# Kernel optimization log

Hardware: AMD Instinct MI355X
Metric: run time of the kernel (lower is better)

The kernel has to match this reference:

```python
import jax, jax.numpy as jnp
import numpy as np

N_NODES = 50000
N_EDGES = 150000
NODE_F, EDGE_F = 4, 11
HID, HID_OUT = 512, 1024
VS, AS_, N_ACT = 2048, 2048, 1000


def _graph_conv(x, W, b, src, dst, n, edge_weight=None):
    # DGL GraphConv, norm='both': D_out^{-1/2} on src feats, sum-aggregate, D_in^{-1/2} on dst.
    deg_out = jnp.maximum(jnp.zeros((n,), x.dtype).at[src].add(1.0), 1.0)
    deg_in = jnp.maximum(jnp.zeros((n,), x.dtype).at[dst].add(1.0), 1.0)
    h = x * (deg_out[:, None] ** -0.5)
    mult_first = W.shape[0] > W.shape[1]
    if mult_first:
        h = h @ W
    m = h[src]  # [E, d] gather
    if edge_weight is not None:
        m = m * edge_weight  # elementwise u_mul_e
    agg = jax.ops.segment_sum(m, dst, num_segments=n)
    if not mult_first:
        agg = agg @ W
    return agg * (deg_in[:, None] ** -0.5) + b


def setup_inputs() -> dict:
    key = jax.random.key(0)
    ks = jax.random.split(key, 16)
    s = 0.05
    return {
        'node_feats': jax.random.normal(ks[0], (N_NODES, NODE_F), jnp.float32),
        'edge_feats': jax.random.normal(ks[1], (N_EDGES, EDGE_F), jnp.float32),
        'W1': jax.random.normal(ks[2], (NODE_F, EDGE_F), jnp.float32) * s,
        'b1': jnp.zeros((EDGE_F,), jnp.float32),
        'W2': jax.random.normal(ks[3], (EDGE_F, HID), jnp.float32) * s,
        'b2': jnp.zeros((HID,), jnp.float32),
        'W3': jax.random.normal(ks[4], (HID, HID_OUT), jnp.float32) * s,
        'b3': jnp.zeros((HID_OUT,), jnp.float32),
        'Wv1': jax.random.normal(ks[5], (HID_OUT, VS), jnp.float32) * s,
        'bv1': jnp.zeros((VS,), jnp.float32),
        'Wv2': jax.random.normal(ks[6], (VS, 1), jnp.float32) * s,
        'bv2': jnp.zeros((1,), jnp.float32),
        'Wa1': jax.random.normal(ks[7], (HID_OUT, AS_), jnp.float32) * s,
        'ba1': jnp.zeros((AS_,), jnp.float32),
        'Wa2': jax.random.normal(ks[8], (AS_, N_ACT), jnp.float32) * s,
        'ba2': jnp.zeros((N_ACT,), jnp.float32),
        'src': jax.random.randint(ks[9], (N_EDGES,), 0, N_NODES, jnp.int32),
        'dst': jax.random.randint(ks[10], (N_EDGES,), 0, N_NODES, jnp.int32),
    }


def reference(node_feats, edge_feats, W1, b1, W2, b2, W3, b3,
              Wv1, bv1, Wv2, bv2, Wa1, ba1, Wa2, ba2, src, dst):
    n = node_feats.shape[0]
    loop = jnp.arange(n, dtype=src.dtype)
    srcL = jnp.concatenate([src, loop])  # add_self_loop
    dstL = jnp.concatenate([dst, loop])
    # self-loop edges get zero edge features (DGL default)
    ef = jnp.concatenate([edge_feats, jnp.zeros((n, edge_feats.shape[1]), edge_feats.dtype)], axis=0)

    h = jax.nn.relu(_graph_conv(node_feats, W1, b1, srcL, dstL, n))          # [N, 11]
    h = jax.nn.relu(_graph_conv(h, W2, b2, srcL, dstL, n, edge_weight=ef))   # [N, 512]
    h = _graph_conv(h, W3, b3, srcL, dstL, n)                                # [N, 1024]

    g_emb = jnp.mean(h, axis=0, keepdims=True)  # dgl.mean_nodes, single graph -> [1, 1024]

    v = jax.nn.relu(g_emb @ Wv1 + bv1) @ Wv2 + bv2        # [1, 1]
    a = jax.nn.relu(g_emb @ Wa1 + ba1) @ Wa2 + ba2        # [1, N_ACT]
    return v + (a - a.mean())
```

## Files before the change

kernel.cpp:

```cpp
#include <hip/hip_runtime.h>

#define NN 50000
#define NE 150000
#define NB 196

__global__ __launch_bounds__(256) void k_deg(const int* __restrict__ src,
                                             const int* __restrict__ dst,
                                             int* __restrict__ deg_out,
                                             int* __restrict__ deg_in) {
    int e = blockIdx.x * 256 + threadIdx.x;
    if (e < NE) {
        atomicAdd(&deg_out[src[e]], 1);
        atomicAdd(&deg_in[dst[e]], 1);
    }
}

__global__ __launch_bounds__(256) void k_bsum(const int* __restrict__ deg_in,
                                              int* __restrict__ bsum_in) {
    __shared__ int si[256];
    int t = threadIdx.x;
    int idx = blockIdx.x * 256 + t;
    si[t] = (idx < NN) ? deg_in[idx] : 0;
    __syncthreads();
    for (int off = 128; off >= 1; off >>= 1) {
        if (t < off) si[t] += si[t + off];
        __syncthreads();
    }
    if (t == 0) bsum_in[blockIdx.x] = si[0];
}

__global__ __launch_bounds__(256) void k_rowptr(const int* __restrict__ deg_in,
                                                const int* __restrict__ deg_out,
                                                const int* __restrict__ bsum_in,
                                                const float* __restrict__ x,
                                                int* __restrict__ rp_in,
                                                float* __restrict__ dins,
                                                float* __restrict__ douts,
                                                float4* __restrict__ xs4) {
    __shared__ int si[256];
    int b = blockIdx.x, t = threadIdx.x;
    si[t] = (t < b) ? bsum_in[t] : 0;
    __syncthreads();
    for (int off = 128; off >= 1; off >>= 1) {
        if (t < off) si[t] += si[t + off];
        __syncthreads();
    }
    int off_in = si[0];
    __syncthreads();
    int idx = b * 256 + t;
    int di = (idx < NN) ? deg_in[idx] : 0;
    si[t] = di;
    __syncthreads();
    for (int off = 1; off < 256; off <<= 1) {
        int a = (t >= off) ? si[t - off] : 0;
        __syncthreads();
        si[t] += a;
        __syncthreads();
    }
    if (idx < NN) {
        rp_in[idx] = off_in + si[t] - di;
        float dif = rsqrtf((float)(di + 1));
        float dqf = rsqrtf((float)(deg_out[idx] + 1));
        dins[idx] = dif;
        douts[idx] = dqf;
        float4 x4 = ((const float4*)x)[idx];
        x4.x *= dqf; x4.y *= dqf; x4.z *= dqf; x4.w *= dqf;
        xs4[idx] = x4;
    }
    if (b == 0 && t == 0) rp_in[NN] = NE;
}

__global__ __launch_bounds__(256) void k_scatter(const int* __restrict__ src,
                                                 const int* __restrict__ dst,
                                                 const float* __restrict__ ef,
                                                 const int* __restrict__ rp_in,
                                                 const float* __restrict__ dins,
                                                 int* __restrict__ cur_in,
                                                 int2* __restrict__ ndcsr,
                                                 float4* __restrict__ ef4,
                                                 float* __restrict__ c) {
    int e = blockIdx.x * 256 + threadIdx.x;
    if (e >= NE) return;
    int s = src[e], d = dst[e];
    int pi = rp_in[d] + atomicAdd(&cur_in[d], 1);
    ndcsr[pi] = make_int2(s, d);
    const float* er = ef + (size_t)e * 11;
    ef4[(size_t)pi * 3 + 0] = make_float4(er[0], er[1], er[2], er[3]);
    ef4[(size_t)pi * 3 + 1] = make_float4(er[4], er[5], er[6], er[7]);
    ef4[(size_t)pi * 3 + 2] = make_float4(er[8], er[9], er[10], 0.f);
    atomicAdd(&c[s], dins[d]);
}

__global__ __launch_bounds__(256) void k_conv1g(const float4* __restrict__ xs4,
                                                const int2* __restrict__ ndcsr,
                                                const int* __restrict__ rp_in,
                                                const float* __restrict__ dins,
                                                const float* __restrict__ douts,
                                                const float* __restrict__ W1,
                                                const float* __restrict__ b1,
                                                float4* __restrict__ h1s4) {
    int n = blockIdx.x * 256 + threadIdx.x;
    if (n >= NN) return;
    float din  = dins[n];
    float dout = douts[n];
    float4 a = xs4[n];
    int beg = rp_in[n], end = rp_in[n + 1];
    for (int p = beg; p < end; p++) {
        float4 xs = xs4[ndcsr[p].x];
        a.x += xs.x; a.y += xs.y; a.z += xs.z; a.w += xs.w;
    }
    float y[12];
    #pragma unroll
    for (int j = 0; j < 11; j++) {
        float t2 = a.x * W1[0 * 11 + j] + a.y * W1[1 * 11 + j] +
                   a.z * W1[2 * 11 + j] + a.w * W1[3 * 11 + j];
        y[j] = fmaxf(fmaf(t2, din, b1[j]), 0.f) * dout;
    }
    y[11] = 0.f;
    h1s4[(size_t)n * 3 + 0] = make_float4(y[0], y[1], y[2],  y[3]);
    h1s4[(size_t)n * 3 + 1] = make_float4(y[4], y[5], y[6],  y[7]);
    h1s4[(size_t)n * 3 + 2] = make_float4(y[8], y[9], y[10], y[11]);
}

#define G2 98
__global__ __launch_bounds__(256) void k_conv2f(const float4* __restrict__ h1s4,
                                                const float4* __restrict__ ef4,
                                                const int2* __restrict__ ndcsr,
                                                const int* __restrict__ rp_in,
                                                const float* __restrict__ c,
                                                const float* __restrict__ dins,
                                                const float* __restrict__ douts,
                                                const float* __restrict__ W2,
                                                const float* __restrict__ b2,
                                                float* __restrict__ t_pad) {
    __shared__ float tile[G2 * 12];
    __shared__ float din_sh[G2], w_sh[G2];
    int tid = threadIdx.x;
    int n0 = blockIdx.x * G2;
    int nend = (n0 + G2 < NN) ? n0 + G2 : NN;
    for (int i = tid; i < G2 * 12; i += 256) tile[i] = 0.f;
    if (tid < G2) {
        int n = n0 + tid;
        if (n < NN) {
            float din = dins[n];
            din_sh[tid] = din;
            w_sh[tid]   = (c[n] + din) * douts[n] * (1.0f / NN);
        } else { din_sh[tid] = 0.f; w_sh[tid] = 0.f; }
    }
    __syncthreads();
    int pbeg = rp_in[n0], pend = rp_in[nend];
    for (int p = pbeg + tid; p < pend; p += 256) {
        int2 sd = ndcsr[p];
        float4 ha = h1s4[(size_t)sd.x * 3 + 0];
        float4 hb = h1s4[(size_t)sd.x * 3 + 1];
        float4 hc = h1s4[(size_t)sd.x * 3 + 2];
        float4 ea = ef4[(size_t)p * 3 + 0];
        float4 eb = ef4[(size_t)p * 3 + 1];
        float4 ec = ef4[(size_t)p * 3 + 2];
        float* row = &tile[(sd.y - n0) * 12];
        atomicAdd(&row[0],  ha.x * ea.x);
        atomicAdd(&row[1],  ha.y * ea.y);
        atomicAdd(&row[2],  ha.z * ea.z);
        atomicAdd(&row[3],  ha.w * ea.w);
        atomicAdd(&row[4],  hb.x * eb.x);
        atomicAdd(&row[5],  hb.y * eb.y);
        atomicAdd(&row[6],  hb.z * eb.z);
        atomicAdd(&row[7],  hb.w * eb.w);
        atomicAdd(&row[8],  hc.x * ec.x);
        atomicAdd(&row[9],  hc.y * ec.y);
        atomicAdd(&row[10], hc.z * ec.z);
    }
    __syncthreads();
    int ch0 = tid, ch1 = tid + 256;
    float w0[11], w1[11];
    #pragma unroll
    for (int j = 0; j < 11; j++) { w0[j] = W2[j * 512 + ch0]; w1[j] = W2[j * 512 + ch1]; }
    float b0 = b2[ch0], b1v = b2[ch1];
    float acc0 = 0.f, acc1 = 0.f;
    int cnt = nend - n0;
    for (int i = 0; i < cnt; i++) {
        const float4* trow = (const float4*)&tile[i * 12];
        float4 ta = trow[0], tb = trow[1], tc = trow[2];
        float din = din_sh[i], wn = w_sh[i];
        float dot0 = ta.x * w0[0] + ta.y * w0[1] + ta.z * w0[2] + ta.w * w0[3] +
                     tb.x * w0[4] + tb.y * w0[5] + tb.z * w0[6] + tb.w * w0[7] +
                     tc.x * w0[8] + tc.y * w0[9] + tc.z * w0[10];
        float dot1 = ta.x * w1[0] + ta.y * w1[1] + ta.z * w1[2] + ta.w * w1[3] +
                     tb.x * w1[4] + tb.y * w1[5] + tb.z * w1[6] + tb.w * w1[7] +
                     tc.x * w1[8] + tc.y * w1[9] + tc.z * w1[10];
        acc0 = fmaf(wn, fmaxf(fmaf(dot0, din, b0),  0.f), acc0);
        acc1 = fmaf(wn, fmaxf(fmaf(dot1, din, b1v), 0.f), acc1);
    }
    atomicAdd(&t_pad[ch0 * 16], acc0);
    atomicAdd(&t_pad[ch1 * 16], acc1);
}

__global__ __launch_bounds__(256) void k_g(const float* __restrict__ t_pad,
                                           const float* __restrict__ W3,
                                           const float* __restrict__ b3,
                                           float* __restrict__ g_pad) {
    int b = blockIdx.x;
    int oc = b & 3, kc = b >> 2;
    int o = oc * 256 + threadIdx.x;
    int k0 = kc * 16;
    __shared__ float ts[16];
    if (threadIdx.x < 16) ts[threadIdx.x] = t_pad[(k0 + threadIdx.x) * 16];
    __syncthreads();
    float acc = (kc == 0) ? b3[o] : 0.f;
    #pragma unroll
    for (int k = 0; k < 16; k++) acc = fmaf(ts[k], W3[(size_t)(k0 + k) * 1024 + o], acc);
    atomicAdd(&g_pad[o * 16], acc);
}

__global__ __launch_bounds__(256) void k_heads1(const float* __restrict__ g_pad,
                                                const float* __restrict__ Wv1,
                                                const float* __restrict__ Wa1,
                                                float* __restrict__ hv_pad,
                                                float* __restrict__ ha_pad) {
    int b = blockIdx.x;
    int oc = b >> 5, kc = b & 31;
    int idx = oc * 256 + threadIdx.x;
    int k0 = kc * 32;
    __shared__ float gs[32];
    if (threadIdx.x < 32) gs[threadIdx.x] = g_pad[(k0 + threadIdx.x) * 16];
    __syncthreads();
    const float* W; float* outp; int o;
    if (idx < 2048) { W = Wv1; outp = hv_pad; o = idx; }
    else            { W = Wa1; outp = ha_pad; o = idx - 2048; }
    float acc = 0.f;
    #pragma unroll 8
    for (int k = 0; k < 32; k++) acc = fmaf(gs[k], W[(size_t)(k0 + k) * 2048 + o], acc);
    atomicAdd(&outp[o * 16], acc);
}

__global__ __launch_bounds__(256) void k_heads2(const float* __restrict__ hv_pad,
                                                const float* __restrict__ bv1,
                                                const float* __restrict__ ha_pad,
                                                const float* __restrict__ ba1,
                                                const float* __restrict__ Wv2,
                                                const float* __restrict__ bv2,
                                                const float* __restrict__ Wa2,
                                                float* __restrict__ a_pad,
                                                float* __restrict__ v) {
    int b = blockIdx.x;
    int tid = threadIdx.x;
    if (b < 256) {
        int oc = b >> 6, kc = b & 63;
        int k0 = kc * 32;
        __shared__ float hs[32];
        if (tid < 32) hs[tid] = fmaxf(ha_pad[(k0 + tid) * 16] + ba1[k0 + tid], 0.f);
        __syncthreads();
        int o = oc * 256 + tid;
        if (o < 1000) {
            float acc = 0.f;
            #pragma unroll 8
            for (int k = 0; k < 32; k++)
                acc = fmaf(hs[k], Wa2[(size_t)(k0 + k) * 1000 + o], acc);
            atomicAdd(&a_pad[o * 16], acc);
        }
    } else {
        __shared__ float red[256];
        float acc = 0.f;
        for (int k = tid; k < 2048; k += 256)
            acc = fmaf(fmaxf(hv_pad[k * 16] + bv1[k], 0.f), Wv2[k], acc);
        red[tid] = acc;
        __syncthreads();
        for (int s = 128; s >= 1; s >>= 1) {
            if (tid < s) red[tid] += red[tid + s];
            __syncthreads();
        }
        if (tid == 0) *v = red[0] + bv2[0];
    }
}

__global__ __launch_bounds__(1024) void k_final(const float* __restrict__ a_pad,
                                                const float* __restrict__ ba2,
                                                const float* __restrict__ vptr,
                                                float* __restrict__ out) {
    __shared__ float red[1024];
    int tid = threadIdx.x;
    float ai = (tid < 1000) ? a_pad[tid * 16] + ba2[tid] : 0.f;
    red[tid] = ai;
    __syncthreads();
    for (int s = 512; s >= 1; s >>= 1) {
        if (tid < s) red[tid] += red[tid + s];
        __syncthreads();
    }
    float amean = red[0] * (1.0f / 1000.0f);
    if (tid < 1000) out[tid] = vptr[0] + ai - amean;
}

extern "C" void kernel_launch(void* const* d_in, const int* in_sizes, int n_in,
                              void* d_out, int out_size, void* d_ws, size_t ws_size,
                              hipStream_t stream) {
    const float* x   = (const float*)d_in[0];
    const float* ef  = (const float*)d_in[1];
    const float* W1  = (const float*)d_in[2];
    const float* b1  = (const float*)d_in[3];
    const float* W2  = (const float*)d_in[4];
    const float* b2  = (const float*)d_in[5];
    const float* W3  = (const float*)d_in[6];
    const float* b3  = (const float*)d_in[7];
    const float* Wv1 = (const float*)d_in[8];
    const float* bv1 = (const float*)d_in[9];
    const float* Wv2 = (const float*)d_in[10];
    const float* bv2 = (const float*)d_in[11];
    const float* Wa1 = (const float*)d_in[12];
    const float* ba1 = (const float*)d_in[13];
    const float* Wa2 = (const float*)d_in[14];
    const float* ba2 = (const float*)d_in[15];
    const int*   src = (const int*)d_in[16];
    const int*   dst = (const int*)d_in[17];
    float* out = (float*)d_out;

    char* ws = (char*)d_ws;
    size_t off = 0;
    auto alloc = [&](size_t bytes) -> void* {
        void* p = ws + off;
        off = (off + bytes + 255) & ~(size_t)255;
        return p;
    };
    int*   deg_out = (int*)  alloc(NN * 4);
    int*   deg_in  = (int*)  alloc(NN * 4);
    int*   cur_in  = (int*)  alloc(NN * 4);
    float* c       = (float*)alloc(NN * 4);
    float* t_pad   = (float*)alloc(512 * 16 * 4);
    float* g_pad   = (float*)alloc(1024 * 16 * 4);
    float* hv_pad  = (float*)alloc(2048 * 16 * 4);
    float* ha_pad  = (float*)alloc(2048 * 16 * 4);
    float* a_pad   = (float*)alloc(1024 * 16 * 4);
    size_t zero_bytes = off;
    int*    bsum_in  = (int*)   alloc(NB * 4);
    int*    rp_in    = (int*)   alloc((NN + 1) * 4);
    float*  dins     = (float*) alloc(NN * 4);
    float*  douts    = (float*) alloc(NN * 4);
    float4* xs4      = (float4*)alloc((size_t)NN * 16);
    int2*   ndcsr    = (int2*)  alloc((size_t)NE * 8);
    float4* ef4      = (float4*)alloc((size_t)NE * 48);
    float4* h1s4     = (float4*)alloc((size_t)NN * 48);
    float*  v        = (float*) alloc(256);

    hipMemsetAsync(d_ws, 0, zero_bytes, stream);

    k_deg<<<(NE + 255) / 256, 256, 0, stream>>>(src, dst, deg_out, deg_in);
    k_bsum<<<NB, 256, 0, stream>>>(deg_in, bsum_in);
    k_rowptr<<<NB, 256, 0, stream>>>(deg_in, deg_out, bsum_in, x, rp_in, dins, douts, xs4);
    k_scatter<<<(NE + 255) / 256, 256, 0, stream>>>(src, dst, ef, rp_in, dins,
                                                    cur_in, ndcsr, ef4, c);
    k_conv1g<<<(NN + 255) / 256, 256, 0, stream>>>(xs4, ndcsr, rp_in, dins, douts,
                                                   W1, b1, h1s4);
    k_conv2f<<<(NN + G2 - 1) / G2, 256, 0, stream>>>(h1s4, ef4, ndcsr, rp_in, c,
                                                     dins, douts, W2, b2, t_pad);
    k_g<<<128, 256, 0, stream>>>(t_pad, W3, b3, g_pad);
    k_heads1<<<512, 256, 0, stream>>>(g_pad, Wv1, Wa1, hv_pad, ha_pad);
    k_heads2<<<257, 256, 0, stream>>>(hv_pad, bv1, ha_pad, ba1, Wv2, bv2, Wa2, a_pad, v);
    k_final<<<1, 1024, 0, stream>>>(a_pad, ba2, v, out);
}
```

Before: 209.6 us.

## Fuse whole pipeline into one cooperative persistent kernel with grid syncs

Replaces the memset and ten separate kernel launches with a single cooperative kernel of 256 blocks by 512 threads. The stages are separated by grid.sync(), and the workspace is zeroed inside the kernel. This removes per-launch overhead and inter-kernel gaps. In exchange, parallelism per stage is capped at 256 resident blocks, the conv2 tile loop now iterates per block with 512 threads, and there are about ten grid-wide barriers. The old multi-kernel path is kept as a fallback if the cooperative launch fails.

```diff
diff --git a/kernel.cpp b/kernel.cpp
--- a/kernel.cpp
+++ b/kernel.cpp
@@ -1,8 +1,268 @@
 #include <hip/hip_runtime.h>
+#include <hip/hip_cooperative_groups.h>
+
+namespace cg = cooperative_groups;
 
 #define NN 50000
 #define NE 150000
+#define NBLK 256
+#define NTHR 512
+#define NG (NBLK * NTHR)
+#define NB2 98
+#define G2 98
+#define NT2 ((NN + G2 - 1) / G2)
 #define NB 196
+
+struct MArgs {
+    const float *x, *ef, *W1, *b1, *W2, *b2, *W3, *b3;
+    const float *Wv1, *bv1, *Wv2, *bv2, *Wa1, *ba1, *Wa2, *ba2;
+    const int *src, *dst;
+    float *out;
+    int *deg_out, *deg_in, *cur_in, *bsum, *rp_in;
+    float *c, *t_pad, *g_pad, *hv_pad, *ha_pad, *a_pad;
+    float *dins, *douts, *v;
+    float4 *xs4, *ef4, *h1s4;
+    int2 *ndcsr;
+    uint4 *zbase;
+    int zcount;
+};
+
+__global__ __launch_bounds__(NTHR, 1) void k_mega(MArgs A) {
+    cg::grid_group grid = cg::this_grid();
+    const int tid = threadIdx.x;
+    const int bid = blockIdx.x;
+    const int gid = bid * NTHR + tid;
+
+    __shared__ float smem[G2 * 12 + 2 * G2 + 16];
+
+    for (int i = gid; i < A.zcount; i += NG) A.zbase[i] = make_uint4(0, 0, 0, 0);
+    grid.sync();
+
+    for (int e = gid; e < NE; e += NG) {
+        atomicAdd(&A.deg_out[A.src[e]], 1);
+        atomicAdd(&A.deg_in[A.dst[e]], 1);
+    }
+    grid.sync();
+
+    if (bid < NB2) {
+        int idx = bid * NTHR + tid;
+        int d = (idx < NN) ? A.deg_in[idx] : 0;
+        int* si = (int*)smem;
+        si[tid] = d;
+        __syncthreads();
+        for (int off = 256; off >= 1; off >>= 1) {
+            if (tid < off) si[tid] += si[tid + off];
+            __syncthreads();
+        }
+        if (tid == 0) A.bsum[bid] = si[0];
+    }
+    grid.sync();
+
+    if (bid < NB2) {
+        int* si = (int*)smem;
+        si[tid] = (tid < bid) ? A.bsum[tid] : 0;
+        __syncthreads();
+        for (int off = 256; off >= 1; off >>= 1) {
+            if (tid < off) si[tid] += si[tid + off];
+            __syncthreads();
+        }
+        int off_in = si[0];
+        __syncthreads();
+        int idx = bid * NTHR + tid;
+        int di = (idx < NN) ? A.deg_in[idx] : 0;
+        si[tid] = di;
+        __syncthreads();
+        for (int off = 1; off < NTHR; off <<= 1) {
+            int a = (tid >= off) ? si[tid - off] : 0;
+            __syncthreads();
+            si[tid] += a;
+            __syncthreads();
+        }
+        if (idx < NN) {
+            A.rp_in[idx] = off_in + si[tid] - di;
+            float dif = rsqrtf((float)(di + 1));
+            float dqf = rsqrtf((float)(A.deg_out[idx] + 1));
+            A.dins[idx] = dif;
+            A.douts[idx] = dqf;
+            float4 x4 = ((const float4*)A.x)[idx];
+            x4.x *= dqf; x4.y *= dqf; x4.z *= dqf; x4.w *= dqf;
+            A.xs4[idx] = x4;
+        }
+        if (bid == 0 && tid == 0) A.rp_in[NN] = NE;
+    }
+    grid.sync();
+
+    for (int e = gid; e < NE; e += NG) {
+        int s = A.src[e], d = A.dst[e];
+        int pi = A.rp_in[d] + atomicAdd(&A.cur_in[d], 1);
+        A.ndcsr[pi] = make_int2(s, d);
+        const float* er = A.ef + (size_t)e * 11;
+        A.ef4[(size_t)pi * 3 + 0] = make_float4(er[0], er[1], er[2], er[3]);
+        A.ef4[(size_t)pi * 3 + 1] = make_float4(er[4], er[5], er[6], er[7]);
+        A.ef4[(size_t)pi * 3 + 2] = make_float4(er[8], er[9], er[10], 0.f);
+        atomicAdd(&A.c[s], A.dins[d]);
+    }
+    grid.sync();
+
+    for (int n = gid; n < NN; n += NG) {
+        float din = A.dins[n], dout = A.douts[n];
+        float4 a = A.xs4[n];
+        int beg = A.rp_in[n], end = A.rp_in[n + 1];
+        for (int p = beg; p < end; p++) {
+            float4 xs = A.xs4[A.ndcsr[p].x];
+            a.x += xs.x; a.y += xs.y; a.z += xs.z; a.w += xs.w;
+        }
+        float y[12];
+        #pragma unroll
+        for (int j = 0; j < 11; j++) {
+            float t2 = a.x * A.W1[0 * 11 + j] + a.y * A.W1[1 * 11 + j] +
+                       a.z * A.W1[2 * 11 + j] + a.w * A.W1[3 * 11 + j];
+            y[j] = fmaxf(fmaf(t2, din, A.b1[j]), 0.f) * dout;
+        }
+        y[11] = 0.f;
+        A.h1s4[(size_t)n * 3 + 0] = make_float4(y[0], y[1], y[2],  y[3]);
+        A.h1s4[(size_t)n * 3 + 1] = make_float4(y[4], y[5], y[6],  y[7]);
+        A.h1s4[(size_t)n * 3 + 2] = make_float4(y[8], y[9], y[10], y[11]);
+    }
+    grid.sync();
+
+    {
+        float* tile   = smem;
+        float* din_sh = smem + G2 * 12;
+        float* w_sh   = smem + G2 * 12 + G2;
+        float w[11];
+        #pragma unroll
+        for (int j = 0; j < 11; j++) w[j] = A.W2[j * 512 + tid];
+        float bias = A.b2[tid];
+        float accT = 0.f;
+        for (int t2 = bid; t2 < NT2; t2 += NBLK) {
+            __syncthreads();
+            int n0 = t2 * G2;
+            int nend = (n0 + G2 < NN) ? n0 + G2 : NN;
+            for (int i = tid; i < G2 * 12; i += NTHR) tile[i] = 0.f;
+            if (tid < G2) {
+                int n = n0 + tid;
+                if (n < NN) {
+                    float din = A.dins[n];
+                    din_sh[tid] = din;
+                    w_sh[tid]   = (A.c[n] + din) * A.douts[n] * (1.0f / NN);
+                } else { din_sh[tid] = 0.f; w_sh[tid] = 0.f; }
+            }
+            __syncthreads();
+            int pbeg = A.rp_in[n0], pend = A.rp_in[nend];
+            for (int p = pbeg + tid; p < pend; p += NTHR) {
+                int2 sd = A.ndcsr[p];
+                float4 ha = A.h1s4[(size_t)sd.x * 3 + 0];
+                float4 hb = A.h1s4[(size_t)sd.x * 3 + 1];
+                float4 hc = A.h1s4[(size_t)sd.x * 3 + 2];
+                float4 ea = A.ef4[(size_t)p * 3 + 0];
+                float4 eb = A.ef4[(size_t)p * 3 + 1];
+                float4 ec = A.ef4[(size_t)p * 3 + 2];
+                float* row = &tile[(sd.y - n0) * 12];
+                atomicAdd(&row[0],  ha.x * ea.x);
+                atomicAdd(&row[1],  ha.y * ea.y);
+                atomicAdd(&row[2],  ha.z * ea.z);
+                atomicAdd(&row[3],  ha.w * ea.w);
+                atomicAdd(&row[4],  hb.x * eb.x);
+                atomicAdd(&row[5],  hb.y * eb.y);
+                atomicAdd(&row[6],  hb.z * eb.z);
+                atomicAdd(&row[7],  hb.w * eb.w);
+                atomicAdd(&row[8],  hc.x * ec.x);
+                atomicAdd(&row[9],  hc.y * ec.y);
+                atomicAdd(&row[10], hc.z * ec.z);
+            }
+            __syncthreads();
+            int cnt = nend - n0;
+            for (int i = 0; i < cnt; i++) {
+                const float4* tr = (const float4*)&tile[i * 12];
+                float4 ta = tr[0], tb = tr[1], tc = tr[2];
+                float dot = ta.x * w[0] + ta.y * w[1] + ta.z * w[2] + ta.w * w[3] +
+                            tb.x * w[4] + tb.y * w[5] + tb.z * w[6] + tb.w * w[7] +
+                            tc.x * w[8] + tc.y * w[9] + tc.z * w[10];
+                accT = fmaf(w_sh[i], fmaxf(fmaf(dot, din_sh[i], bias), 0.f), accT);
+            }
+        }
+        atomicAdd(&A.t_pad[tid * 16], accT);
+    }
+    grid.sync();
+
+    if (bid < 32) {
+        int oc = bid & 1, kc = bid >> 1;
+        int o = oc * NTHR + tid;
+        int k0 = kc * 32;
+        float* ts = smem;
+        if (tid < 32) ts[tid] = A.t_pad[(k0 + tid) * 16];
+        __syncthreads();
+        float acc = (kc == 0) ? A.b3[o] : 0.f;
+        #pragma unroll
+        for (int k = 0; k < 32; k++) acc = fmaf(ts[k], A.W3[(size_t)(k0 + k) * 1024 + o], acc);
+        atomicAdd(&A.g_pad[o * 16], acc);
+    }
+    grid.sync();
+
+    if (bid < 128) {
+        int oc = bid >> 4, kc = bid & 15;
+        int idx = oc * NTHR + tid;
+        int k0 = kc * 64;
+        float* gs = smem;
+        if (tid < 64) gs[tid] = A.g_pad[(k0 + tid) * 16];
+        __syncthreads();
+        const float* W; float* outp; int o;
+        if (idx < 2048) { W = A.Wv1; outp = A.hv_pad; o = idx; }
+        else            { W = A.Wa1; outp = A.ha_pad; o = idx - 2048; }
+        float acc = 0.f;
+        #pragma unroll 8
+        for (int k = 0; k < 64; k++) acc = fmaf(gs[k], W[(size_t)(k0 + k) * 2048 + o], acc);
+        atomicAdd(&outp[o * 16], acc);
+    }
+    grid.sync();
+
+    if (bid < 64) {
+        int oc = bid & 1, kc = bid >> 1;
+        int k0 = kc * 64;
+        float* hs = smem;
+        if (tid < 64) hs[tid] = fmaxf(A.ha_pad[(k0 + tid) * 16] + A.ba1[k0 + tid], 0.f);
+        __syncthreads();
+        int o = oc * NTHR + tid;
+        if (o < 1000) {
+            float acc = 0.f;
+            #pragma unroll 8
+            for (int k = 0; k < 64; k++)
+                acc = fmaf(hs[k], A.Wa2[(size_t)(k0 + k) * 1000 + o], acc);
+            atomicAdd(&A.a_pad[o * 16], acc);
+        }
+    } else if (bid == 64) {
+        float* red = smem;
+        float acc = 0.f;
+        for (int k = tid; k < 2048; k += NTHR)
+            acc = fmaf(fmaxf(A.hv_pad[k * 16] + A.bv1[k], 0.f), A.Wv2[k], acc);
+        red[tid] = acc;
+        __syncthreads();
+        for (int s2 = 256; s2 >= 1; s2 >>= 1) {
+            if (tid < s2) red[tid] += red[tid + s2];
+            __syncthreads();
+        }
+        if (tid == 0) A.v[0] = red[0] + A.bv2[0];
+    }
+    grid.sync();
+
+    if (bid == 0) {
+        float* red = smem;
+        float a0 = (tid < 1000) ? A.a_pad[tid * 16] + A.ba2[tid] : 0.f;
+        int i1 = tid + NTHR;
+        float a1 = (i1 < 1000) ? A.a_pad[i1 * 16] + A.ba2[i1] : 0.f;
+        red[tid] = a0 + a1;
+        __syncthreads();
+        for (int s2 = 256; s2 >= 1; s2 >>= 1) {
+            if (tid < s2) red[tid] += red[tid + s2];
+            __syncthreads();
+        }
+        float amean = red[0] * (1.0f / 1000.0f);
+        float vv = A.v[0];
+        if (tid < 1000) A.out[tid] = vv + a0 - amean;
+        if (i1 < 1000)  A.out[i1]  = vv + a1 - amean;
+    }
+}
 
 __global__ __launch_bounds__(256) void k_deg(const int* __restrict__ src,
                                              const int* __restrict__ dst,
@@ -122,7 +382,6 @@
     h1s4[(size_t)n * 3 + 2] = make_float4(y[8], y[9], y[10], y[11]);
 }
 
-#define G2 98
 __global__ __launch_bounds__(256) void k_conv2f(const float4* __restrict__ h1s4,
                                                 const float4* __restrict__ ef4,
                                                 const int2* __restrict__ ndcsr,
@@ -330,7 +589,7 @@
     float* ha_pad  = (float*)alloc(2048 * 16 * 4);
     float* a_pad   = (float*)alloc(1024 * 16 * 4);
     size_t zero_bytes = off;
-    int*    bsum_in  = (int*)   alloc(NB * 4);
+    int*    bsum     = (int*)   alloc(NB * 4);
     int*    rp_in    = (int*)   alloc((NN + 1) * 4);
     float*  dins     = (float*) alloc(NN * 4);
     float*  douts    = (float*) alloc(NN * 4);
@@ -340,19 +599,34 @@
     float4* h1s4     = (float4*)alloc((size_t)NN * 48);
     float*  v        = (float*) alloc(256);
 
-    hipMemsetAsync(d_ws, 0, zero_bytes, stream);
-
-    k_deg<<<(NE + 255) / 256, 256, 0, stream>>>(src, dst, deg_out, deg_in);
-    k_bsum<<<NB, 256, 0, stream>>>(deg_in, bsum_in);
-    k_rowptr<<<NB, 256, 0, stream>>>(deg_in, deg_out, bsum_in, x, rp_in, dins, douts, xs4);
-    k_scatter<<<(NE + 255) / 256, 256, 0, stream>>>(src, dst, ef, rp_in, dins,
-                                                    cur_in, ndcsr, ef4, c);
-    k_conv1g<<<(NN + 255) / 256, 256, 0, stream>>>(xs4, ndcsr, rp_in, dins, douts,
-                                                   W1, b1, h1s4);
-    k_conv2f<<<(NN + G2 - 1) / G2, 256, 0, stream>>>(h1s4, ef4, ndcsr, rp_in, c,
-                                                     dins, douts, W2, b2, t_pad);
-    k_g<<<128, 256, 0, stream>>>(t_pad, W3, b3, g_pad);
-    k_heads1<<<512, 256, 0, stream>>>(g_pad, Wv1, Wa1, hv_pad, ha_pad);
-    k_heads2<<<257, 256, 0, stream>>>(hv_pad, bv1, ha_pad, ba1, Wv2, bv2, Wa2, a_pad, v);
-    k_final<<<1, 1024, 0, stream>>>(a_pad, ba2, v, out);
-}
+    MArgs A;
+    A.x = x; A.ef = ef; A.W1 = W1; A.b1 = b1; A.W2 = W2; A.b2 = b2; A.W3 = W3; A.b3 = b3;
+    A.Wv1 = Wv1; A.bv1 = bv1; A.Wv2 = Wv2; A.bv2 = bv2;
+    A.Wa1 = Wa1; A.ba1 = ba1; A.Wa2 = Wa2; A.ba2 = ba2;
+    A.src = src; A.dst = dst; A.out = out;
+    A.deg_out = deg_out; A.deg_in = deg_in; A.cur_in = cur_in; A.bsum = bsum; A.rp_in = rp_in;
+    A.c = c; A.t_pad = t_pad; A.g_pad = g_pad; A.hv_pad = hv_pad; A.ha_pad = ha_pad; A.a_pad = a_pad;
+    A.dins = dins; A.douts = douts; A.v = v;
+    A.xs4 = xs4; A.ef4 = ef4; A.h1s4 = h1s4; A.ndcsr = ndcsr;
+    A.zbase = (uint4*)d_ws; A.zcount = (int)(zero_bytes / 16);
+
+    void* kargs[] = { &A };
+    hipError_t err = hipLaunchCooperativeKernel((void*)k_mega, dim3(NBLK), dim3(NTHR),
+                                                kargs, 0, stream);
+    if (err != hipSuccess) {
+        hipMemsetAsync(d_ws, 0, zero_bytes, stream);
+        k_deg<<<(NE + 255) / 256, 256, 0, stream>>>(src, dst, deg_out, deg_in);
+        k_bsum<<<NB, 256, 0, stream>>>(deg_in, bsum);
+        k_rowptr<<<NB, 256, 0, stream>>>(deg_in, deg_out, bsum, x, rp_in, dins, douts, xs4);
+        k_scatter<<<(NE + 255) / 256, 256, 0, stream>>>(src, dst, ef, rp_in, dins,
+                                                        cur_in, ndcsr, ef4, c);
+        k_conv1g<<<(NN + 255) / 256, 256, 0, stream>>>(xs4, ndcsr, rp_in, dins, douts,
+                                                       W1, b1, h1s4);
+        k_conv2f<<<NT2, 256, 0, stream>>>(h1s4, ef4, ndcsr, rp_in, c,
+                                          dins, douts, W2, b2, t_pad);
+        k_g<<<128, 256, 0, stream>>>(t_pad, W3, b3, g_pad);
+        k_heads1<<<512, 256, 0, stream>>>(g_pad, Wv1, Wa1, hv_pad, ha_pad);
+        k_heads2<<<257, 256, 0, stream>>>(hv_pad, bv1, ha_pad, ba1, Wv2, bv2, Wa2, a_pad, v);
+        k_final<<<1, 1024, 0, stream>>>(a_pad, ba2, v, out);
+    }
+}
```

After: 505.5 us. 141% more time.

## Accumulate conv2 edge messages in registers per thread chunk, use unsafe float atomics

Applied to the files above, without the earlier changes.

In the conv2 kernel, each thread now handles a contiguous chunk of CSR edges and sums messages for the same destination in registers. It flushes to the shared tile only when the destination changes, so far fewer LDS atomics are issued. The node tile size doubles from 98 to 196, which halves the grid and the per-block W2 reduction work but lowers parallelism. All float atomicAdds are switched to unsafeAtomicAdd so the hardware float-atomic instructions are used instead of CAS loops.

```diff
diff --git a/kernel.cpp b/kernel.cpp
--- a/kernel.cpp
+++ b/kernel.cpp
@@ -3,6 +3,8 @@
 #define NN 50000
 #define NE 150000
 #define NB 196
+#define G2 196
+#define NT2 ((NN + G2 - 1) / G2)
 
 __global__ __launch_bounds__(256) void k_deg(const int* __restrict__ src,
                                              const int* __restrict__ dst,
@@ -88,7 +90,7 @@
     ef4[(size_t)pi * 3 + 0] = make_float4(er[0], er[1], er[2], er[3]);
     ef4[(size_t)pi * 3 + 1] = make_float4(er[4], er[5], er[6], er[7]);
     ef4[(size_t)pi * 3 + 2] = make_float4(er[8], er[9], er[10], 0.f);
-    atomicAdd(&c[s], dins[d]);
+    unsafeAtomicAdd(&c[s], dins[d]);
 }
 
 __global__ __launch_bounds__(256) void k_conv1g(const float4* __restrict__ xs4,
@@ -122,7 +124,6 @@
     h1s4[(size_t)n * 3 + 2] = make_float4(y[8], y[9], y[10], y[11]);
 }
 
-#define G2 98
 __global__ __launch_bounds__(256) void k_conv2f(const float4* __restrict__ h1s4,
                                                 const float4* __restrict__ ef4,
                                                 const int2* __restrict__ ndcsr,
@@ -149,26 +150,46 @@
     }
     __syncthreads();
     int pbeg = rp_in[n0], pend = rp_in[nend];
-    for (int p = pbeg + tid; p < pend; p += 256) {
+    int range = pend - pbeg;
+    int chunk = (range + 255) >> 8;
+    int p0 = pbeg + tid * chunk;
+    int p1 = p0 + chunk; if (p1 > pend) p1 = pend;
+    float acc[11];
+    int cur = -1;
+    for (int p = p0; p < p1; p++) {
         int2 sd = ndcsr[p];
+        if (sd.y != cur) {
+            if (cur >= 0) {
+                float* row = &tile[(cur - n0) * 12];
+                #pragma unroll
+                for (int j = 0; j < 11; j++) unsafeAtomicAdd(&row[j], acc[j]);
+            }
+            cur = sd.y;
+            #pragma unroll
+            for (int j = 0; j < 11; j++) acc[j] = 0.f;
+        }
         float4 ha = h1s4[(size_t)sd.x * 3 + 0];
         float4 hb = h1s4[(size_t)sd.x * 3 + 1];
         float4 hc = h1s4[(size_t)sd.x * 3 + 2];
         float4 ea = ef4[(size_t)p * 3 + 0];
         float4 eb = ef4[(size_t)p * 3 + 1];
         float4 ec = ef4[(size_t)p * 3 + 2];
-        float* row = &tile[(sd.y - n0) * 12];
-        atomicAdd(&row[0],  ha.x * ea.x);
-        atomicAdd(&row[1],  ha.y * ea.y);
-        atomicAdd(&row[2],  ha.z * ea.z);
-        atomicAdd(&row[3],  ha.w * ea.w);
-        atomicAdd(&row[4],  hb.x * eb.x);
-        atomicAdd(&row[5],  hb.y * eb.y);
-        atomicAdd(&row[6],  hb.z * eb.z);
-        atomicAdd(&row[7],  hb.w * eb.w);
-        atomicAdd(&row[8],  hc.x * ec.x);
-        atomicAdd(&row[9],  hc.y * ec.y);
-        atomicAdd(&row[10], hc.z * ec.z);
+        acc[0]  = fmaf(ha.x, ea.x, acc[0]);
+        acc[1]  = fmaf(ha.y, ea.y, acc[1]);
+        acc[2]  = fmaf(ha.z, ea.z, acc[2]);
+        acc[3]  = fmaf(ha.w, ea.w, acc[3]);
+        acc[4]  = fmaf(hb.x, eb.x, acc[4]);
+        acc[5]  = fmaf(hb.y, eb.y, acc[5]);
+        acc[6]  = fmaf(hb.z, eb.z, acc[6]);
+        acc[7]  = fmaf(hb.w, eb.w, acc[7]);
+        acc[8]  = fmaf(hc.x, ec.x, acc[8]);
+        acc[9]  = fmaf(hc.y, ec.y, acc[9]);
+        acc[10] = fmaf(hc.w == 0.f ? hc.z : hc.z, ec.z, acc[10]);
+    }
+    if (cur >= 0) {
+        float* row = &tile[(cur - n0) * 12];
+        #pragma unroll
+        for (int j = 0; j < 11; j++) unsafeAtomicAdd(&row[j], acc[j]);
     }
     __syncthreads();
     int ch0 = tid, ch1 = tid + 256;
@@ -191,8 +212,8 @@
         acc0 = fmaf(wn, fmaxf(fmaf(dot0, din, b0),  0.f), acc0);
         acc1 = fmaf(wn, fmaxf(fmaf(dot1, din, b1v), 0.f), acc1);
     }
-    atomicAdd(&t_pad[ch0 * 16], acc0);
-    atomicAdd(&t_pad[ch1 * 16], acc1);
+    unsafeAtomicAdd(&t_pad[ch0 * 16], acc0);
+    unsafeAtomicAdd(&t_pad[ch1 * 16], acc1);
 }
 
 __global__ __launch_bounds__(256) void k_g(const float* __restrict__ t_pad,
@@ -209,7 +230,7 @@
     float acc = (kc == 0) ? b3[o] : 0.f;
     #pragma unroll
     for (int k = 0; k < 16; k++) acc = fmaf(ts[k], W3[(size_t)(k0 + k) * 1024 + o], acc);
-    atomicAdd(&g_pad[o * 16], acc);
+    unsafeAtomicAdd(&g_pad[o * 16], acc);
 }
 
 __global__ __launch_bounds__(256) void k_heads1(const float* __restrict__ g_pad,
@@ -230,7 +251,7 @@
     float acc = 0.f;
     #pragma unroll 8
     for (int k = 0; k < 32; k++) acc = fmaf(gs[k], W[(size_t)(k0 + k) * 2048 + o], acc);
-    atomicAdd(&outp[o * 16], acc);
+    unsafeAtomicAdd(&outp[o * 16], acc);
 }
 
 __global__ __launch_bounds__(256) void k_heads2(const float* __restrict__ hv_pad,
@@ -256,7 +277,7 @@
             #pragma unroll 8
             for (int k = 0; k < 32; k++)
                 acc = fmaf(hs[k], Wa2[(size_t)(k0 + k) * 1000 + o], acc);
-            atomicAdd(&a_pad[o * 16], acc);
+            unsafeAtomicAdd(&a_pad[o * 16], acc);
         }
     } else {
         __shared__ float red[256];
@@ -330,7 +351,7 @@
     float* ha_pad  = (float*)alloc(2048 * 16 * 4);
     float* a_pad   = (float*)alloc(1024 * 16 * 4);
     size_t zero_bytes = off;
-    int*    bsum_in  = (int*)   alloc(NB * 4);
+    int*    bsum     = (int*)   alloc(NB * 4);
     int*    rp_in    = (int*)   alloc((NN + 1) * 4);
     float*  dins     = (float*) alloc(NN * 4);
     float*  douts    = (float*) alloc(NN * 4);
@@ -343,14 +364,14 @@
     hipMemsetAsync(d_ws, 0, zero_bytes, stream);
 
     k_deg<<<(NE + 255) / 256, 256, 0, stream>>>(src, dst, deg_out, deg_in);
-    k_bsum<<<NB, 256, 0, stream>>>(deg_in, bsum_in);
-    k_rowptr<<<NB, 256, 0, stream>>>(deg_in, deg_out, bsum_in, x, rp_in, dins, douts, xs4);
+    k_bsum<<<NB, 256, 0, stream>>>(deg_in, bsum);
+    k_rowptr<<<NB, 256, 0, stream>>>(deg_in, deg_out, bsum, x, rp_in, dins, douts, xs4);
     k_scatter<<<(NE + 255) / 256, 256, 0, stream>>>(src, dst, ef, rp_in, dins,
                                                     cur_in, ndcsr, ef4, c);
     k_conv1g<<<(NN + 255) / 256, 256, 0, stream>>>(xs4, ndcsr, rp_in, dins, douts,
                                                    W1, b1, h1s4);
-    k_conv2f<<<(NN + G2 - 1) / G2, 256, 0, stream>>>(h1s4, ef4, ndcsr, rp_in, c,
-                                                     dins, douts, W2, b2, t_pad);
+    k_conv2f<<<NT2, 256, 0, stream>>>(h1s4, ef4, ndcsr, rp_in, c,
+                                      dins, douts, W2, b2, t_pad);
     k_g<<<128, 256, 0, stream>>>(t_pad, W3, b3, g_pad);
     k_heads1<<<512, 256, 0, stream>>>(g_pad, Wv1, Wa1, hv_pad, ha_pad);
     k_heads2<<<257, 256, 0, stream>>>(hv_pad, bv1, ha_pad, ba1, Wv2, bv2, Wa2, a_pad, v);
```

New measurement: 212.2 us. Within noise of the previous version (+1.3%).
